# Optimization experiments

Hardware: AMD Instinct MI355X
Metric: run time of the kernel (lower is better)

Reference implementation:

```python
import jax, jax.numpy as jnp
import numpy as np

K = 4          # neighbors
R = 2          # step_ratio
O = 64         # output_size


def setup_inputs() -> dict:
    key = jax.random.key(0)
    ks = jax.random.split(key, 7)
    B, C, N = 16, 128, 2048
    x = jax.random.normal(ks[0], (B, C, N), jnp.float32)
    # 1x1 conv weights stored as [out, in]; bias [out]
    w1 = jax.random.normal(ks[1], (O, 2 * C), jnp.float32) * (1.0 / np.sqrt(2 * C))
    b1 = jax.random.normal(ks[2], (O,), jnp.float32) * 0.01
    w2 = jax.random.normal(ks[3], (O * R, 2 * C + O), jnp.float32) * (1.0 / np.sqrt(2 * C + O))
    b2 = jax.random.normal(ks[4], (O * R,), jnp.float32) * 0.01
    w3 = jax.random.normal(ks[5], (O, O), jnp.float32) * (1.0 / np.sqrt(O))
    b3 = jax.random.normal(ks[6], (O,), jnp.float32) * 0.01
    return {"x": x, "w1": w1, "b1": b1, "w2": w2, "b2": b2, "w3": w3, "b3": b3}


def _knn_idx(x, k):
    # x: [B, C, N]; returns indices of k nearest neighbors (incl. self) [B, N, k]
    inner = -2.0 * jnp.einsum('bcn,bcm->bnm', x, x)           # [B, N, N]
    xx = jnp.sum(x * x, axis=1)                                # [B, N]
    pd = -xx[:, :, None] - inner - xx[:, None, :]              # negative sq dist
    return jax.lax.top_k(pd, k)[1]                             # [B, N, k]


def _graph_feature(x, k):
    # minus_center=False variant used by EF_expansion
    idx = _knn_idx(x, k)                                       # [B, N, k]
    xt = jnp.transpose(x, (0, 2, 1))                           # [B, N, C]
    feat = jax.vmap(lambda xb, ib: xb[ib])(xt, idx)            # [B, N, k, C]
    center = jnp.broadcast_to(xt[:, :, None, :], feat.shape)   # [B, N, k, C]
    f = jnp.concatenate([center, feat], axis=3)                # [B, N, k, 2C]
    return jnp.transpose(f, (0, 3, 1, 2))                      # [B, 2C, N, k]


def _conv1x1(w, b, x):
    # x: [B, Cin, H, W] -> [B, Cout, H, W]
    return jnp.einsum('oc,bchw->bohw', w, x) + b[None, :, None, None]


def reference(x, w1, b1, w2, b2, w3, b3):
    B, C, N = x.shape
    ief = jnp.transpose(_graph_feature(x, K), (0, 1, 3, 2))    # [B, 2C, k, N]
    e1 = _conv1x1(w1, b1, ief)                                 # [B, O, k, N]
    e = jax.nn.relu(jnp.concatenate([e1, ief], axis=1))        # [B, O+2C, k, N]
    e2 = jax.nn.relu(_conv1x1(w2, b2, e))                      # [B, O*R, k, N]
    # [B,O*R,k,N] -> [B,k,N,O*R] -> [B,k,N*R,O] -> [B,O,k,N*R]
    e2 = jnp.transpose(e2, (0, 2, 3, 1)).reshape(B, K, N * R, O)
    e2 = jnp.transpose(e2, (0, 3, 1, 2))
    e3 = _conv1x1(w3, b3, e2)                                  # [B, O, k, N*R]
    return jnp.max(e3, axis=2)                                 # [B, O, N*R]
```

## Files before the change

kernel.cpp:

```cpp
#include <hip/hip_runtime.h>
#include <cstdint>
#include <cstddef>

#define B_  16
#define C_  128
#define N_  2048
#define K_  4
#define O_  64
#define C2_ 256
#define ED_ 320
#define NM_ 4096

typedef float  f32x4  __attribute__((ext_vector_type(4)));
typedef short  s16x8  __attribute__((ext_vector_type(8)));
typedef __bf16 bf16x4 __attribute__((ext_vector_type(4)));
typedef __bf16 bf16x8 __attribute__((ext_vector_type(8)));
typedef unsigned short u16;
typedef unsigned int   u32;
typedef unsigned int   u32x4 __attribute__((ext_vector_type(4)));

__device__ __forceinline__ u32 umin32(u32 a, u32 b) { return a < b ? a : b; }
__device__ __forceinline__ u32 umax32(u32 a, u32 b) { return a > b ? a : b; }

__device__ __forceinline__ s16x8 ldw_bf16(const float* __restrict__ p) {
  float4 a = *(const float4*)p;
  float4 c = *(const float4*)(p + 4);
  bf16x8 r;
  r[0] = (__bf16)a.x; r[1] = (__bf16)a.y; r[2] = (__bf16)a.z; r[3] = (__bf16)a.w;
  r[4] = (__bf16)c.x; r[5] = (__bf16)c.y; r[6] = (__bf16)c.z; r[7] = (__bf16)c.w;
  return __builtin_bit_cast(s16x8, r);
}

__device__ __forceinline__ u32 relu2(u32 u) {
  u32 s = u & 0x80008000u;
  u32 m = s - (s >> 15);
  return u & ~(m | s);
}

__device__ __forceinline__ s16x8 relu8(s16x8 v) {
  u32x4 u = __builtin_bit_cast(u32x4, v);
  u[0] = relu2(u[0]); u[1] = relu2(u[1]);
  u[2] = relu2(u[2]); u[3] = relu2(u[3]);
  return __builtin_bit_cast(s16x8, u);
}

__device__ __forceinline__ void glds16(const void* g, void* l) {
  __builtin_amdgcn_global_load_lds(
      (const __attribute__((address_space(1))) u32*)g,
      (__attribute__((address_space(3))) u32*)l, 16, 0, 0);
}

__global__ __launch_bounds__(256) void prep_kernel(const float* __restrict__ x,
                                                   const float* __restrict__ w1,
                                                   const float* __restrict__ w2,
                                                   const float* __restrict__ w3,
                                                   float* __restrict__ xT32,
                                                   u16* __restrict__ xh,
                                                   float* __restrict__ xx,
                                                   u16* __restrict__ wh) {
  const int t = threadIdx.x;
  if (blockIdx.y == B_) {
    const int gid = blockIdx.x * 256 + t;
    for (int i = gid; i < 15360; i += 8192) {
      const float* src; u16* dst;
      if (i < 4096)       { src = w1 + (size_t)i * 4;            dst = wh + (size_t)i * 4; }
      else if (i < 14336) { src = w2 + (size_t)(i - 4096) * 4;   dst = wh + 16384 + (size_t)(i - 4096) * 4; }
      else                { src = w3 + (size_t)(i - 14336) * 4;  dst = wh + 57344 + (size_t)(i - 14336) * 4; }
      float4 v = *(const float4*)src;
      ushort4 h;
      h.x = __builtin_bit_cast(u16, (__bf16)v.x);
      h.y = __builtin_bit_cast(u16, (__bf16)v.y);
      h.z = __builtin_bit_cast(u16, (__bf16)v.z);
      h.w = __builtin_bit_cast(u16, (__bf16)v.w);
      *(ushort4*)dst = h;
    }
    return;
  }

  __shared__ __align__(16) float sx[C_][65];
  const int b = blockIdx.y, n0 = blockIdx.x * 64;
  const float* xb = x + (size_t)b * C_ * N_;
  for (int u = t; u < C_ * 16; u += 256) {
    int c = u >> 4, f4 = u & 15;
    float4 v = *(const float4*)&xb[(size_t)c * N_ + n0 + f4 * 4];
    sx[c][f4 * 4 + 0] = v.x; sx[c][f4 * 4 + 1] = v.y;
    sx[c][f4 * 4 + 2] = v.z; sx[c][f4 * 4 + 3] = v.w;
  }
  __syncthreads();
  if (t < 64) {
    float s = 0.f;
    for (int c = 0; c < C_; ++c) { float v = sx[c][t]; s = fmaf(v, v, s); }
    xx[b * N_ + n0 + t] = s;
  }
  for (int u = t; u < 64 * 16; u += 256) {
    int n = u >> 4, cb = u & 15;
    float vv[8]; s16x8 hv;
#pragma unroll
    for (int j = 0; j < 8; ++j) {
      float v = sx[cb * 8 + j][n];
      vv[j] = v;
      hv[j] = (short)__builtin_bit_cast(u16, (__bf16)v);
    }
    size_t ro = ((size_t)b * N_ + n0 + n) * C_;
    *(float4*)&xT32[ro + cb * 8]     = make_float4(vv[0], vv[1], vv[2], vv[3]);
    *(float4*)&xT32[ro + cb * 8 + 4] = make_float4(vv[4], vv[5], vv[6], vv[7]);
    int sc = cb ^ (n & 7);
    *(s16x8*)&xh[ro + sc * 8] = hv;
  }
}

__global__ __launch_bounds__(256) void knn_mfma(const u16* __restrict__ xh,
                                                const float* __restrict__ xx,
                                                int* __restrict__ cand8) {
  __shared__ __align__(16) char smem[40960];
  const int b = blockIdx.y, q0 = blockIdx.x * 64;
  const int t = threadIdx.x;
  const int lane = t & 63, wv = t >> 6, lq = t & 15, lh = (t >> 4) & 3;
  const u16* xhb = xh + (size_t)b * N_ * C_;
  const float* xxb = xx + b * N_;

  s16x8 qf[4][4];
#pragma unroll
  for (int qt = 0; qt < 4; ++qt)
#pragma unroll
    for (int ks = 0; ks < 4; ++ks) {
      int q = q0 + qt * 16 + lq;
      int ch = (ks * 4 + lh) ^ (q & 7);
      qf[qt][ks] = *(const s16x8*)&xhb[(size_t)q * C_ + ch * 8];
    }

  u32 pk[4][5];
#pragma unroll
  for (int qt = 0; qt < 4; ++qt)
#pragma unroll
    for (int s = 0; s < 5; ++s) pk[qt][s] = 0xFFFFFFFFu;

  auto stage = [&](int bufi, int m0) {
    const char* s = (const char*)(xhb + (size_t)m0 * C_);
    char* d = smem + bufi * 16384;
#pragma unroll
    for (int c = 0; c < 4; ++c) {
      int off = (wv * 4 + c) * 1024;
      glds16(s + off + lane * 16, d + off);
    }
  };

  stage(0, 0);
  asm volatile("s_waitcnt vmcnt(0)");
  __syncthreads();

  for (int step = 0; step < 32; ++step) {
    const int cur = step & 1;
    if (step < 31) stage(cur ^ 1, (step + 1) * 64);
    const char* mb = smem + cur * 16384;
    f32x4 acc[4];
#pragma unroll
    for (int qt = 0; qt < 4; ++qt) acc[qt] = (f32x4){0.f, 0.f, 0.f, 0.f};
#pragma unroll
    for (int ks = 0; ks < 4; ++ks) {
      int row = wv * 16 + lq;
      int ch = (ks * 4 + lh) ^ (lq & 7);
      s16x8 mf = *(const s16x8*)(mb + row * 256 + ch * 16);
#pragma unroll
      for (int qt = 0; qt < 4; ++qt)
        acc[qt] = __builtin_amdgcn_mfma_f32_16x16x32_bf16(mf, qf[qt][ks], acc[qt], 0, 0, 0);
    }
    const int mrow = step * 64 + wv * 16 + lh * 4;
    float4 xm4 = *(const float4*)&xxb[mrow];
    float xma[4] = {xm4.x, xm4.y, xm4.z, xm4.w};
#pragma unroll
    for (int r = 0; r < 4; ++r) {
#pragma unroll
      for (int qt = 0; qt < 4; ++qt) {
        float dd = fmaf(acc[qt][r], -2.f, xma[r]);
        u32 s = __builtin_bit_cast(u32, dd);
        u32 neg = (u32)((int)s >> 31);
        u32 u = s ^ (neg | 0x80000000u);
        u32 v = (u & 0xFFFFF800u) | (u32)(mrow + r);
#pragma unroll
        for (int s5 = 0; s5 < 5; ++s5) {
          u32 lo = umin32(v, pk[qt][s5]);
          v = umax32(v, pk[qt][s5]);
          pk[qt][s5] = lo;
        }
      }
    }
    asm volatile("s_waitcnt vmcnt(0)");
    __syncthreads();
  }

  u32* cd = (u32*)smem;
  const int unit = wv * 4 + lh;
#pragma unroll
  for (int qt = 0; qt < 4; ++qt) {
    int ql = qt * 16 + lq;
#pragma unroll
    for (int s = 0; s < 5; ++s) cd[ql * 85 + unit * 5 + s] = pk[qt][s];
  }
  __syncthreads();
  if (t < 64) {
    u32 fd[8];
#pragma unroll
    for (int s = 0; s < 8; ++s) fd[s] = 0xFFFFFFFFu;
    for (int j = 0; j < 80; ++j) {
      u32 v = cd[t * 85 + j];
#pragma unroll
      for (int s = 0; s < 8; ++s) {
        u32 lo = umin32(v, fd[s]);
        v = umax32(v, fd[s]);
        fd[s] = lo;
      }
    }
#pragma unroll
    for (int s = 0; s < 8; ++s)
      cand8[((size_t)b * N_ + q0 + t) * 8 + s] = (int)(fd[s] & 0x7FFu);
  }
}

__global__ __launch_bounds__(256) void rerank_kernel(const float* __restrict__ xT32,
                                                     const float* __restrict__ xx,
                                                     const int* __restrict__ cand8,
                                                     int* __restrict__ knn_out) {
  __shared__ __align__(16) float sq[64][132];
  __shared__ float sd[64][8];
  __shared__ int   si[64][8];
  const int b = blockIdx.y, n0 = blockIdx.x * 64;
  const int t = threadIdx.x;
  const float* xb32 = xT32 + (size_t)b * N_ * C_;
  for (int u = t; u < 64 * 32; u += 256) {
    int n = u >> 5, seg = u & 31;
    *(float4*)&sq[n][seg * 4] = *(const float4*)&xb32[(size_t)(n0 + n) * C_ + seg * 4];
  }
  __syncthreads();
  const int ql = t >> 2, cs = t & 3;
#pragma unroll
  for (int cc = 0; cc < 2; ++cc) {
    int cslot = cs + cc * 4;
    int idx = cand8[((size_t)b * N_ + n0 + ql) * 8 + cslot];
    const float* mr = &xb32[(size_t)idx * C_];
    float a0 = 0.f, a1 = 0.f, a2 = 0.f, a3 = 0.f;
#pragma unroll 8
    for (int i = 0; i < 32; ++i) {
      float4 qv = *(const float4*)&sq[ql][i * 4];
      float4 mv = *(const float4*)&mr[i * 4];
      a0 = fmaf(qv.x, mv.x, a0); a1 = fmaf(qv.y, mv.y, a1);
      a2 = fmaf(qv.z, mv.z, a2); a3 = fmaf(qv.w, mv.w, a3);
    }
    float dot = (a0 + a1) + (a2 + a3);
    sd[ql][cslot] = xx[(size_t)b * N_ + idx] - 2.f * dot;
    si[ql][cslot] = idx;
  }
  __syncthreads();
  if (t < 64) {
    float dloc[8]; int iloc[8];
#pragma unroll
    for (int j = 0; j < 8; ++j) { dloc[j] = sd[t][j]; iloc[j] = si[t][j]; }
    u32 used = 0;
#pragma unroll
    for (int s = 0; s < 4; ++s) {
      float bdv = 1e30f; int bidx = 0x7fffffff; int bj = 0;
#pragma unroll
      for (int j = 0; j < 8; ++j) {
        if (!((used >> j) & 1)) {
          bool bet = (dloc[j] < bdv) || (dloc[j] == bdv && iloc[j] < bidx);
          if (bet) { bdv = dloc[j]; bidx = iloc[j]; bj = j; }
        }
      }
      used |= 1u << bj;
      knn_out[((size_t)b * N_ + n0 + t) * K_ + s] = bidx;
    }
  }
}

__global__ __launch_bounds__(256) void xx_kernel(const float* __restrict__ x,
                                                 float* __restrict__ xx) {
  int g = blockIdx.x * 256 + threadIdx.x;
  int b = g >> 11;
  int n = g & (N_ - 1);
  const float* xp = x + (size_t)b * C_ * N_ + n;
  float s = 0.f;
#pragma unroll 8
  for (int c = 0; c < C_; ++c) { float v = xp[(size_t)c * N_]; s += v * v; }
  xx[g] = s;
}

__global__ __launch_bounds__(256) void knn_kernel(const float* __restrict__ x,
                                                  const float* __restrict__ xx,
                                                  int* __restrict__ knn_out) {
  __shared__ __align__(16) float qT[C_ * 64];
  __shared__ __align__(16) float mT[C_ * 64];
  const int b = blockIdx.y;
  const int q0 = blockIdx.x * 64;
  const int t = threadIdx.x;
  const float* xb = x + (size_t)b * C_ * N_;
  const float* xxb = xx + b * N_;
  for (int i = t; i < C_ * 64; i += 256) {
    int c = i >> 6, q = i & 63;
    qT[i] = xb[(size_t)c * N_ + q0 + q];
  }
  const int tq = t & 15;
  const int tm = t >> 4;
  float bd[4][4]; int bi[4][4];
#pragma unroll
  for (int a = 0; a < 4; ++a)
#pragma unroll
    for (int s = 0; s < 4; ++s) { bd[a][s] = 1e30f; bi[a][s] = 0; }
  for (int m0 = 0; m0 < N_; m0 += 64) {
    __syncthreads();
    for (int i = t; i < C_ * 64; i += 256) {
      int c = i >> 6, m = i & 63;
      mT[i] = xb[(size_t)c * N_ + m0 + m];
    }
    __syncthreads();
    float acc[4][4];
#pragma unroll
    for (int a = 0; a < 4; ++a)
#pragma unroll
      for (int j = 0; j < 4; ++j) acc[a][j] = 0.f;
#pragma unroll 4
    for (int c = 0; c < C_; ++c) {
      float4 qv = *(const float4*)&qT[c * 64 + tq * 4];
      float4 mv = *(const float4*)&mT[c * 64 + tm * 4];
      float qa[4] = {qv.x, qv.y, qv.z, qv.w};
      float ma[4] = {mv.x, mv.y, mv.z, mv.w};
#pragma unroll
      for (int a = 0; a < 4; ++a)
#pragma unroll
        for (int j = 0; j < 4; ++j) acc[a][j] += qa[a] * ma[j];
    }
#pragma unroll
    for (int j = 0; j < 4; ++j) {
      float xm = xxb[m0 + tm * 4 + j];
      int id = m0 + tm * 4 + j;
#pragma unroll
      for (int a = 0; a < 4; ++a) {
        float d = xm - 2.f * acc[a][j];
        if (d < bd[a][3]) {
          bd[a][3] = d; bi[a][3] = id;
#pragma unroll
          for (int s = 3; s > 0; --s)
            if (bd[a][s] < bd[a][s - 1]) {
              float td = bd[a][s]; bd[a][s] = bd[a][s - 1]; bd[a][s - 1] = td;
              int ti = bi[a][s]; bi[a][s] = bi[a][s - 1]; bi[a][s - 1] = ti;
            }
        }
      }
    }
  }
  __syncthreads();
  float* cd = qT;
  int* ci = (int*)mT;
#pragma unroll
  for (int a = 0; a < 4; ++a) {
    int q = tq * 4 + a;
#pragma unroll
    for (int s = 0; s < 4; ++s) {
      cd[q * 64 + tm * 4 + s] = bd[a][s];
      ci[q * 64 + tm * 4 + s] = bi[a][s];
    }
  }
  __syncthreads();
  if (t < 64) {
    float fd[4]; int fi[4];
#pragma unroll
    for (int s = 0; s < 4; ++s) { fd[s] = 1e30f; fi[s] = 0; }
    for (int j = 0; j < 64; ++j) {
      float d = cd[t * 64 + j];
      int id = ci[t * 64 + j];
      if (d < fd[3]) {
        fd[3] = d; fi[3] = id;
#pragma unroll
        for (int s = 3; s > 0; --s)
          if (fd[s] < fd[s - 1]) {
            float td = fd[s]; fd[s] = fd[s - 1]; fd[s - 1] = td;
            int ti = fi[s]; fi[s] = fi[s - 1]; fi[s - 1] = ti;
          }
      }
    }
#pragma unroll
    for (int s = 0; s < 4; ++s)
      knn_out[(b * N_ + q0 + t) * K_ + s] = fi[s];
  }
}

__global__ __launch_bounds__(256, 5) void fused_mfma(
    const float* __restrict__ x, const u16* __restrict__ xh,
    const u16* __restrict__ wh, const int* __restrict__ knn_idx,
    const float* __restrict__ w1, const float* __restrict__ b1,
    const float* __restrict__ w2, const float* __restrict__ b2,
    const float* __restrict__ w3, const float* __restrict__ b3,
    float* __restrict__ out) {
  __shared__ __align__(16) char fsm[30976];
  __bf16 (*cT)[136]  = (__bf16(*)[136])(fsm);
  __bf16 (*e1T)[72]  = (__bf16(*)[72])(fsm + 4352);
  float  (*oSt)[36]  = (float(*)[36])(fsm + 4352);
  __bf16 (*nT)[136]  = (__bf16(*)[136])(fsm + 13568);
  __bf16 (*e2T)[136] = (__bf16(*)[136])(fsm + 13568);

  const int b  = blockIdx.y;
  const int n0 = blockIdx.x * 16;
  const int t  = threadIdx.x;
  const float* xb = x + (size_t)b * C_ * N_;
  const u16* xhb = xh ? xh + (size_t)b * N_ * C_ : nullptr;
  const u16* w1h = wh;
  const u16* w2h = wh + 16384;
  const u16* w3h = wh + 57344;

  {
    const int stn = t >> 4, stc = t & 15;
    const int kbase = (b * N_ + n0) * K_;
    if (xhb) {
      int gn = n0 + stn;
      *(s16x8*)&cT[stn][stc * 8] =
          *(const s16x8*)&xhb[(size_t)gn * C_ + ((stc ^ (gn & 7)) * 8)];
#pragma unroll
      for (int it = 0; it < 4; ++it) {
        int col = stn + 16 * it;
        int nid = knn_idx[kbase + col];
        *(s16x8*)&nT[col][stc * 8] =
            *(const s16x8*)&xhb[(size_t)nid * C_ + ((stc ^ (nid & 7)) * 8)];
      }
    } else {
      const float* srcc = xb + (size_t)(stc * 8) * N_ + n0 + stn;
      bf16x8 raw;
#pragma unroll
      for (int j = 0; j < 8; ++j) raw[j] = (__bf16)srcc[(size_t)j * N_];
      *(bf16x8*)&cT[stn][stc * 8] = raw;
#pragma unroll
      for (int it = 0; it < 4; ++it) {
        int col = stn + 16 * it;
        int nid = knn_idx[kbase + col];
        const float* src = xb + (size_t)(stc * 8) * N_ + nid;
        bf16x8 rw;
#pragma unroll
        for (int j = 0; j < 8; ++j) rw[j] = (__bf16)src[(size_t)j * N_];
        *(bf16x8*)&nT[col][stc * 8] = rw;
      }
    }
  }
  __syncthreads();

  const int lq = t & 15;
  const int lh = (t >> 4) & 3;
  const int wv = t >> 6;

  {
    const u16* w1hr = w1h + (size_t)(wv * 16 + lq) * C2_;
    const float* w1r = w1 + (size_t)(wv * 16 + lq) * C2_;
    f32x4 acc[4];
#pragma unroll
    for (int cg = 0; cg < 4; ++cg) acc[cg] = (f32x4){0.f, 0.f, 0.f, 0.f};
#pragma unroll
    for (int ks = 0; ks < 8; ++ks) {
      s16x8 a = wh ? *(const s16x8*)&w1hr[ks * 32 + lh * 8]
                   : ldw_bf16(w1r + ks * 32 + lh * 8);
#pragma unroll
      for (int cg = 0; cg < 4; ++cg) {
        const __bf16* bp = (ks < 4)
            ? &cT[cg * 4 + (lq >> 2)][ks * 32 + lh * 8]
            : &nT[cg * 16 + lq][(ks - 4) * 32 + lh * 8];
        acc[cg] = __builtin_amdgcn_mfma_f32_16x16x32_bf16(
            a, *(const s16x8*)bp, acc[cg], 0, 0, 0);
      }
    }
#pragma unroll
    for (int cg = 0; cg < 4; ++cg) {
      bf16x4 st;
#pragma unroll
      for (int r = 0; r < 4; ++r) {
        float v = acc[cg][r] + b1[wv * 16 + lh * 4 + r];
        st[r] = (__bf16)fmaxf(v, 0.f);
      }
      *(bf16x4*)&e1T[cg * 16 + lq][wv * 16 + lh * 4] = st;
    }
  }
  __syncthreads();

  f32x4 acc2[2][4];
  {
    const u16* w2hr0 = w2h + (size_t)(wv * 32 + lq) * ED_;
    const u16* w2hr1 = w2hr0 + (size_t)16 * ED_;
    const float* w2r0 = w2 + (size_t)(wv * 32 + lq) * ED_;
    const float* w2r1 = w2r0 + (size_t)16 * ED_;
#pragma unroll
    for (int ro = 0; ro < 2; ++ro)
#pragma unroll
      for (int cg = 0; cg < 4; ++cg) acc2[ro][cg] = (f32x4){0.f, 0.f, 0.f, 0.f};
#pragma unroll
    for (int ks = 0; ks < 10; ++ks) {
      s16x8 a0 = wh ? *(const s16x8*)&w2hr0[ks * 32 + lh * 8]
                    : ldw_bf16(w2r0 + ks * 32 + lh * 8);
      s16x8 a1 = wh ? *(const s16x8*)&w2hr1[ks * 32 + lh * 8]
                    : ldw_bf16(w2r1 + ks * 32 + lh * 8);
#pragma unroll
      for (int cg = 0; cg < 4; ++cg) {
        s16x8 bf;
        if (ks < 2)      bf = *(const s16x8*)&e1T[cg * 16 + lq][ks * 32 + lh * 8];
        else if (ks < 6) bf = relu8(*(const s16x8*)&cT[cg * 4 + (lq >> 2)][(ks - 2) * 32 + lh * 8]);
        else             bf = relu8(*(const s16x8*)&nT[cg * 16 + lq][(ks - 6) * 32 + lh * 8]);
        acc2[0][cg] = __builtin_amdgcn_mfma_f32_16x16x32_bf16(a0, bf, acc2[0][cg], 0, 0, 0);
        acc2[1][cg] = __builtin_amdgcn_mfma_f32_16x16x32_bf16(a1, bf, acc2[1][cg], 0, 0, 0);
      }
    }
  }
  __syncthreads();
  {
#pragma unroll
    for (int ro = 0; ro < 2; ++ro)
#pragma unroll
      for (int cg = 0; cg < 4; ++cg) {
        bf16x4 st;
#pragma unroll
        for (int r = 0; r < 4; ++r) {
          float v = acc2[ro][cg][r] + b2[wv * 32 + ro * 16 + lh * 4 + r];
          st[r] = (__bf16)fmaxf(v, 0.f);
        }
        *(bf16x4*)&e2T[cg * 16 + lq][wv * 32 + ro * 16 + lh * 4] = st;
      }
  }
  __syncthreads();

  {
    s16x8 a0, a1;
    if (wh) {
      const u16* w3hr = w3h + (size_t)(wv * 16 + lq) * O_;
      a0 = *(const s16x8*)&w3hr[lh * 8];
      a1 = *(const s16x8*)&w3hr[32 + lh * 8];
    } else {
      const float* w3r = w3 + (size_t)(wv * 16 + lq) * O_;
      a0 = ldw_bf16(w3r + lh * 8);
      a1 = ldw_bf16(w3r + 32 + lh * 8);
    }
#pragma unroll
    for (int cg = 0; cg < 8; ++cg) {
      int col = cg * 16 + lq;
      int nl = col >> 3, rr = (col >> 2) & 1, kk = col & 3;
      const __bf16* base = &e2T[nl * 4 + kk][rr * 64];
      f32x4 acc = {0.f, 0.f, 0.f, 0.f};
      acc = __builtin_amdgcn_mfma_f32_16x16x32_bf16(a0, *(const s16x8*)(base + lh * 8),      acc, 0, 0, 0);
      acc = __builtin_amdgcn_mfma_f32_16x16x32_bf16(a1, *(const s16x8*)(base + 32 + lh * 8), acc, 0, 0, 0);
      float vv[4];
#pragma unroll
      for (int r = 0; r < 4; ++r) {
        float v = acc[r];
        v = fmaxf(v, __shfl_xor(v, 1));
        v = fmaxf(v, __shfl_xor(v, 2));
        vv[r] = v;
      }
      if ((lq & 3) == 0) {
        int mloc = col >> 2;
        int o = wv * 16 + lh * 4;
#pragma unroll
        for (int r = 0; r < 4; ++r) oSt[o + r][mloc] = vv[r] + b3[o + r];
      }
    }
  }
  __syncthreads();

#pragma unroll
  for (int it = 0; it < 2; ++it) {
    int u = t + it * 256;
    int o = u >> 3, seg = u & 7;
    *(float4*)&out[((size_t)b * O_ + o) * NM_ + n0 * 2 + seg * 4] =
        *(const float4*)&oSt[o][seg * 4];
  }
}

extern "C" void kernel_launch(void* const* d_in, const int* in_sizes, int n_in,
                              void* d_out, int out_size, void* d_ws, size_t ws_size,
                              hipStream_t stream) {
  const float* x  = (const float*)d_in[0];
  const float* w1 = (const float*)d_in[1];
  const float* b1 = (const float*)d_in[2];
  const float* w2 = (const float*)d_in[3];
  const float* b2 = (const float*)d_in[4];
  const float* w3 = (const float*)d_in[5];
  const float* b3 = (const float*)d_in[6];
  float* out = (float*)d_out;

  const size_t off_xh   = (size_t)B_ * N_ * C_ * 4;
  const size_t off_xx   = off_xh + (size_t)B_ * N_ * C_ * 2;
  const size_t off_c8   = off_xx + (size_t)B_ * N_ * 4;
  const size_t off_knn  = off_c8 + (size_t)B_ * N_ * 8 * 4;
  const size_t off_wh   = off_knn + (size_t)B_ * N_ * K_ * 4;
  const size_t NEED     = off_wh + (size_t)61440 * 2;

  if (ws_size >= NEED) {
    float* xT32 = (float*)d_ws;
    u16*   xhp  = (u16*)((char*)d_ws + off_xh);
    float* xx   = (float*)((char*)d_ws + off_xx);
    int*   c8   = (int*)((char*)d_ws + off_c8);
    int*   knn  = (int*)((char*)d_ws + off_knn);
    u16*   whp  = (u16*)((char*)d_ws + off_wh);

    hipLaunchKernelGGL(prep_kernel, dim3(N_ / 64, B_ + 1), dim3(256), 0, stream,
                       x, w1, w2, w3, xT32, xhp, xx, whp);
    hipLaunchKernelGGL(knn_mfma, dim3(N_ / 64, B_), dim3(256), 0, stream, xhp, xx, c8);
    hipLaunchKernelGGL(rerank_kernel, dim3(N_ / 64, B_), dim3(256), 0, stream, xT32, xx, c8, knn);
    hipLaunchKernelGGL(fused_mfma, dim3(N_ / 16, B_), dim3(256), 0, stream,
                       x, xhp, whp, knn, w1, b1, w2, b2, w3, b3, out);
  } else {
    float* xx = (float*)d_ws;
    int* knn = (int*)((char*)d_ws + (size_t)B_ * N_ * 4);
    hipLaunchKernelGGL(xx_kernel, dim3((B_ * N_) / 256), dim3(256), 0, stream, x, xx);
    hipLaunchKernelGGL(knn_kernel, dim3(N_ / 64, B_), dim3(256), 0, stream, x, xx, knn);
    hipLaunchKernelGGL(fused_mfma, dim3(N_ / 16, B_), dim3(256), 0, stream,
                       x, (const u16*)nullptr, (const u16*)nullptr, knn,
                       w1, b1, w2, b2, w3, b3, out);
  }
}
```

Baseline: 119.1 us.

## Add persistent tiled fused kernel with register-resident weights and async LDS double buffering

Introduces fused_tiled, where each block handles 64 points in four 16-point iterations. The block loads the bf16 weight fragments for all three convs into registers once, instead of reloading them per 16-point block. Center and neighbor rows are staged into double-buffered LDS with global_load_lds using an XOR swizzle, so the gather for the next tile overlaps compute on the current one. This cuts redundant weight traffic and gather latency, at the cost of heavy register pressure (launch bounds 256,2), more LDS per block, and lower occupancy.

```diff
diff --git a/kernel.cpp b/kernel.cpp
--- a/kernel.cpp
+++ b/kernel.cpp
@@ -10,6 +10,7 @@
 #define C2_ 256
 #define ED_ 320
 #define NM_ 4096
+#define ROWB 256
 
 typedef float  f32x4  __attribute__((ext_vector_type(4)));
 typedef short  s16x8  __attribute__((ext_vector_type(8)));
@@ -36,7 +37,6 @@
   u32 m = s - (s >> 15);
   return u & ~(m | s);
 }
-
 __device__ __forceinline__ s16x8 relu8(s16x8 v) {
   u32x4 u = __builtin_bit_cast(u32x4, v);
   u[0] = relu2(u[0]); u[1] = relu2(u[1]);
@@ -272,6 +272,195 @@
   }
 }
 
+__global__ __launch_bounds__(256, 2) void fused_tiled(
+    const u16* __restrict__ xh, const u16* __restrict__ wh,
+    const int* __restrict__ knn_idx,
+    const float* __restrict__ b1, const float* __restrict__ b2,
+    const float* __restrict__ b3, float* __restrict__ out) {
+  __shared__ __align__(16) char fsm[66560];
+  __bf16* e1T = (__bf16*)(fsm + 40960);
+  float*  oSt = (float*)(fsm + 40960);
+  char*   e2T = fsm + 50176;
+
+  const int t  = threadIdx.x;
+  const int lane = t & 63, wv = t >> 6, lq = t & 15, lh = (t >> 4) & 3;
+  const int b = blockIdx.y;
+  const int nbase = blockIdx.x * 64;
+  const u16* xhb = xh + (size_t)b * N_ * C_;
+  const int kb = (b * N_ + nbase) * K_;
+
+  s16x8 w1f[8], w2f0[10], w2f1[10], w3f[2];
+  {
+    const u16* r1 = wh + (size_t)(wv * 16 + lq) * C2_;
+#pragma unroll
+    for (int ks = 0; ks < 8; ++ks) w1f[ks] = *(const s16x8*)&r1[ks * 32 + lh * 8];
+    const u16* r20 = wh + 16384 + (size_t)(wv * 32 + lq) * ED_;
+    const u16* r21 = r20 + (size_t)16 * ED_;
+#pragma unroll
+    for (int ks = 0; ks < 10; ++ks) {
+      w2f0[ks] = *(const s16x8*)&r20[ks * 32 + lh * 8];
+      w2f1[ks] = *(const s16x8*)&r21[ks * 32 + lh * 8];
+    }
+    const u16* r3 = wh + 57344 + (size_t)(wv * 16 + lq) * O_;
+    w3f[0] = *(const s16x8*)&r3[lh * 8];
+    w3f[1] = *(const s16x8*)&r3[32 + lh * 8];
+  }
+  const float4 b1v  = *(const float4*)&b1[wv * 16 + lh * 4];
+  const float4 b2v0 = *(const float4*)&b2[wv * 32 + lh * 4];
+  const float4 b2v1 = *(const float4*)&b2[wv * 32 + 16 + lh * 4];
+  const float4 b3v  = *(const float4*)&b3[wv * 16 + lh * 4];
+
+  auto stageTile = [&](int it, const int* nids) {
+    char* cb = fsm + (it & 1) * 20480;
+    char* nb = cb + 4096;
+    glds16((const char*)xhb + (size_t)(nbase + it * 16 + wv * 4) * ROWB + lane * 16,
+           cb + wv * 4 * ROWB);
+#pragma unroll
+    for (int g = 0; g < 4; ++g) {
+      int col = wv * 16 + g * 4 + (lane >> 4);
+      int nid = nids[g];
+      int sc = (lane & 15) ^ (col & 7) ^ (nid & 7);
+      glds16((const char*)xhb + (size_t)nid * ROWB + sc * 16,
+             nb + (wv * 16 + g * 4) * ROWB);
+    }
+  };
+
+  int nids[4];
+#pragma unroll
+  for (int g = 0; g < 4; ++g)
+    nids[g] = knn_idx[kb + wv * 16 + g * 4 + (lane >> 4)];
+  stageTile(0, nids);
+
+  for (int it = 0; it < 4; ++it) {
+    if (it < 3) {
+#pragma unroll
+      for (int g = 0; g < 4; ++g)
+        nids[g] = knn_idx[kb + (it + 1) * 64 + wv * 16 + g * 4 + (lane >> 4)];
+    }
+    asm volatile("s_waitcnt vmcnt(0)" ::: "memory");
+    __syncthreads();
+    if (it < 3) stageTile(it + 1, nids);
+
+    const char* cb = fsm + (it & 1) * 20480;
+    const char* nb = cb + 4096;
+
+    {
+      f32x4 acc1[4];
+#pragma unroll
+      for (int cg = 0; cg < 4; ++cg) acc1[cg] = (f32x4){0.f, 0.f, 0.f, 0.f};
+#pragma unroll
+      for (int ks = 0; ks < 8; ++ks) {
+#pragma unroll
+        for (int cg = 0; cg < 4; ++cg) {
+          const char* bp;
+          if (ks < 4) {
+            int r = cg * 4 + (lq >> 2);
+            bp = cb + r * ROWB + (((ks * 4 + lh) ^ (r & 7)) * 16);
+          } else {
+            int r = cg * 16 + lq;
+            bp = nb + r * ROWB + ((((ks - 4) * 4 + lh) ^ (r & 7)) * 16);
+          }
+          acc1[cg] = __builtin_amdgcn_mfma_f32_16x16x32_bf16(
+              w1f[ks], *(const s16x8*)bp, acc1[cg], 0, 0, 0);
+        }
+      }
+      const float bb[4] = {b1v.x, b1v.y, b1v.z, b1v.w};
+#pragma unroll
+      for (int cg = 0; cg < 4; ++cg) {
+        bf16x4 st;
+#pragma unroll
+        for (int r = 0; r < 4; ++r) st[r] = (__bf16)fmaxf(acc1[cg][r] + bb[r], 0.f);
+        *(bf16x4*)&e1T[(cg * 16 + lq) * 72 + wv * 16 + lh * 4] = st;
+      }
+    }
+    __syncthreads();
+
+    {
+      f32x4 acc2[2][4];
+#pragma unroll
+      for (int ro = 0; ro < 2; ++ro)
+#pragma unroll
+        for (int cg = 0; cg < 4; ++cg) acc2[ro][cg] = (f32x4){0.f, 0.f, 0.f, 0.f};
+#pragma unroll
+      for (int ks = 0; ks < 10; ++ks) {
+#pragma unroll
+        for (int cg = 0; cg < 4; ++cg) {
+          s16x8 bf;
+          if (ks < 2) {
+            bf = *(const s16x8*)&e1T[(cg * 16 + lq) * 72 + ks * 32 + lh * 8];
+          } else if (ks < 6) {
+            int r = cg * 4 + (lq >> 2);
+            bf = relu8(*(const s16x8*)(cb + r * ROWB + ((((ks - 2) * 4 + lh) ^ (r & 7)) * 16)));
+          } else {
+            int r = cg * 16 + lq;
+            bf = relu8(*(const s16x8*)(nb + r * ROWB + ((((ks - 6) * 4 + lh) ^ (r & 7)) * 16)));
+          }
+          acc2[0][cg] = __builtin_amdgcn_mfma_f32_16x16x32_bf16(w2f0[ks], bf, acc2[0][cg], 0, 0, 0);
+          acc2[1][cg] = __builtin_amdgcn_mfma_f32_16x16x32_bf16(w2f1[ks], bf, acc2[1][cg], 0, 0, 0);
+        }
+      }
+      const float c0[4] = {b2v0.x, b2v0.y, b2v0.z, b2v0.w};
+      const float c1[4] = {b2v1.x, b2v1.y, b2v1.z, b2v1.w};
+#pragma unroll
+      for (int ro = 0; ro < 2; ++ro)
+#pragma unroll
+        for (int cg = 0; cg < 4; ++cg) {
+          int col = cg * 16 + lq;
+          int e = wv * 32 + ro * 16 + lh * 4;
+          int j = e >> 3, sub = e & 7;
+          int pos = j ^ (col & 7);
+          bf16x4 st;
+#pragma unroll
+          for (int r = 0; r < 4; ++r) {
+            float v = acc2[ro][cg][r] + (ro ? c1[r] : c0[r]);
+            st[r] = (__bf16)fmaxf(v, 0.f);
+          }
+          *(bf16x4*)(e2T + col * ROWB + pos * 16 + sub * 2) = st;
+        }
+    }
+    __syncthreads();
+
+    {
+#pragma unroll
+      for (int cg = 0; cg < 8; ++cg) {
+        int col = cg * 16 + lq;
+        int nl = col >> 3, rr = (col >> 2) & 1, kk = col & 3;
+        int row = nl * 4 + kk;
+        int j1 = rr * 8 + lh, j2 = rr * 8 + 4 + lh;
+        s16x8 f1 = *(const s16x8*)(e2T + row * ROWB + ((j1 ^ (row & 7)) * 16));
+        s16x8 f2 = *(const s16x8*)(e2T + row * ROWB + ((j2 ^ (row & 7)) * 16));
+        f32x4 acc = {0.f, 0.f, 0.f, 0.f};
+        acc = __builtin_amdgcn_mfma_f32_16x16x32_bf16(w3f[0], f1, acc, 0, 0, 0);
+        acc = __builtin_amdgcn_mfma_f32_16x16x32_bf16(w3f[1], f2, acc, 0, 0, 0);
+        float vv[4];
+#pragma unroll
+        for (int r = 0; r < 4; ++r) {
+          float v = acc[r];
+          v = fmaxf(v, __shfl_xor(v, 1));
+          v = fmaxf(v, __shfl_xor(v, 2));
+          vv[r] = v;
+        }
+        if ((lq & 3) == 0) {
+          int mloc = col >> 2;
+          int o = wv * 16 + lh * 4;
+          const float b3a[4] = {b3v.x, b3v.y, b3v.z, b3v.w};
+#pragma unroll
+          for (int r = 0; r < 4; ++r) oSt[(o + r) * 36 + mloc] = vv[r] + b3a[r];
+        }
+      }
+    }
+    __syncthreads();
+
+#pragma unroll
+    for (int io = 0; io < 2; ++io) {
+      int u = t + io * 256;
+      int o = u >> 3, seg = u & 7;
+      *(float4*)&out[((size_t)b * O_ + o) * NM_ + nbase * 2 + it * 32 + seg * 4] =
+          *(const float4*)&oSt[o * 36 + seg * 4];
+    }
+  }
+}
+
 __global__ __launch_bounds__(256) void xx_kernel(const float* __restrict__ x,
                                                  float* __restrict__ xx) {
   int g = blockIdx.x * 256 + threadIdx.x;
@@ -383,9 +572,8 @@
   }
 }
 
-__global__ __launch_bounds__(256, 5) void fused_mfma(
-    const float* __restrict__ x, const u16* __restrict__ xh,
-    const u16* __restrict__ wh, const int* __restrict__ knn_idx,
+__global__ __launch_bounds__(256, 5) void fused_fb(
+    const float* __restrict__ x, const int* __restrict__ knn_idx,
     const float* __restrict__ w1, const float* __restrict__ b1,
     const float* __restrict__ w2, const float* __restrict__ b2,
     const float* __restrict__ w3, const float* __restrict__ b3,
@@ -401,41 +589,24 @@
   const int n0 = blockIdx.x * 16;
   const int t  = threadIdx.x;
   const float* xb = x + (size_t)b * C_ * N_;
-  const u16* xhb = xh ? xh + (size_t)b * N_ * C_ : nullptr;
-  const u16* w1h = wh;
-  const u16* w2h = wh + 16384;
-  const u16* w3h = wh + 57344;
 
   {
     const int stn = t >> 4, stc = t & 15;
     const int kbase = (b * N_ + n0) * K_;
-    if (xhb) {
-      int gn = n0 + stn;
-      *(s16x8*)&cT[stn][stc * 8] =
-          *(const s16x8*)&xhb[(size_t)gn * C_ + ((stc ^ (gn & 7)) * 8)];
-#pragma unroll
-      for (int it = 0; it < 4; ++it) {
-        int col = stn + 16 * it;
-        int nid = knn_idx[kbase + col];
-        *(s16x8*)&nT[col][stc * 8] =
-            *(const s16x8*)&xhb[(size_t)nid * C_ + ((stc ^ (nid & 7)) * 8)];
-      }
-    } else {
-      const float* srcc = xb + (size_t)(stc * 8) * N_ + n0 + stn;
-      bf16x8 raw;
-#pragma unroll
-      for (int j = 0; j < 8; ++j) raw[j] = (__bf16)srcc[(size_t)j * N_];
-      *(bf16x8*)&cT[stn][stc * 8] = raw;
-#pragma unroll
-      for (int it = 0; it < 4; ++it) {
-        int col = stn + 16 * it;
-        int nid = knn_idx[kbase + col];
-        const float* src = xb + (size_t)(stc * 8) * N_ + nid;
-        bf16x8 rw;
-#pragma unroll
-        for (int j = 0; j < 8; ++j) rw[j] = (__bf16)src[(size_t)j * N_];
-        *(bf16x8*)&nT[col][stc * 8] = rw;
-      }
+    const float* srcc = xb + (size_t)(stc * 8) * N_ + n0 + stn;
+    bf16x8 raw;
+#pragma unroll
+    for (int j = 0; j < 8; ++j) raw[j] = (__bf16)srcc[(size_t)j * N_];
+    *(bf16x8*)&cT[stn][stc * 8] = raw;
+#pragma unroll
+    for (int it = 0; it < 4; ++it) {
+      int col = stn + 16 * it;
+      int nid = knn_idx[kbase + col];
+      const float* src = xb + (size_t)(stc * 8) * N_ + nid;
+      bf16x8 rw;
+#pragma unroll
+      for (int j = 0; j < 8; ++j) rw[j] = (__bf16)src[(size_t)j * N_];
+      *(bf16x8*)&nT[col][stc * 8] = rw;
     }
   }
   __syncthreads();
@@ -445,15 +616,13 @@
   const int wv = t >> 6;
 
   {
-    const u16* w1hr = w1h + (size_t)(wv * 16 + lq) * C2_;
     const float* w1r = w1 + (size_t)(wv * 16 + lq) * C2_;
     f32x4 acc[4];
 #pragma unroll
     for (int cg = 0; cg < 4; ++cg) acc[cg] = (f32x4){0.f, 0.f, 0.f, 0.f};
 #pragma unroll
     for (int ks = 0; ks < 8; ++ks) {
-      s16x8 a = wh ? *(const s16x8*)&w1hr[ks * 32 + lh * 8]
-                   : ldw_bf16(w1r + ks * 32 + lh * 8);
+      s16x8 a = ldw_bf16(w1r + ks * 32 + lh * 8);
 #pragma unroll
       for (int cg = 0; cg < 4; ++cg) {
         const __bf16* bp = (ks < 4)
@@ -478,8 +647,6 @@
 
   f32x4 acc2[2][4];
   {
-    const u16* w2hr0 = w2h + (size_t)(wv * 32 + lq) * ED_;
-    const u16* w2hr1 = w2hr0 + (size_t)16 * ED_;
     const float* w2r0 = w2 + (size_t)(wv * 32 + lq) * ED_;
     const float* w2r1 = w2r0 + (size_t)16 * ED_;
 #pragma unroll
@@ -488,10 +655,8 @@
       for (int cg = 0; cg < 4; ++cg) acc2[ro][cg] = (f32x4){0.f, 0.f, 0.f, 0.f};
 #pragma unroll
     for (int ks = 0; ks < 10; ++ks) {
-      s16x8 a0 = wh ? *(const s16x8*)&w2hr0[ks * 32 + lh * 8]
-                    : ldw_bf16(w2r0 + ks * 32 + lh * 8);
-      s16x8 a1 = wh ? *(const s16x8*)&w2hr1[ks * 32 + lh * 8]
-                    : ldw_bf16(w2r1 + ks * 32 + lh * 8);
+      s16x8 a0 = ldw_bf16(w2r0 + ks * 32 + lh * 8);
+      s16x8 a1 = ldw_bf16(w2r1 + ks * 32 + lh * 8);
 #pragma unroll
       for (int cg = 0; cg < 4; ++cg) {
         s16x8 bf;
@@ -521,16 +686,9 @@
   __syncthreads();
 
   {
-    s16x8 a0, a1;
-    if (wh) {
-      const u16* w3hr = w3h + (size_t)(wv * 16 + lq) * O_;
-      a0 = *(const s16x8*)&w3hr[lh * 8];
-      a1 = *(const s16x8*)&w3hr[32 + lh * 8];
-    } else {
-      const float* w3r = w3 + (size_t)(wv * 16 + lq) * O_;
-      a0 = ldw_bf16(w3r + lh * 8);
-      a1 = ldw_bf16(w3r + 32 + lh * 8);
-    }
+    const float* w3r = w3 + (size_t)(wv * 16 + lq) * O_;
+    s16x8 a0 = ldw_bf16(w3r + lh * 8);
+    s16x8 a1 = ldw_bf16(w3r + 32 + lh * 8);
 #pragma unroll
     for (int cg = 0; cg < 8; ++cg) {
       int col = cg * 16 + lq;
@@ -597,15 +755,14 @@
                        x, w1, w2, w3, xT32, xhp, xx, whp);
     hipLaunchKernelGGL(knn_mfma, dim3(N_ / 64, B_), dim3(256), 0, stream, xhp, xx, c8);
     hipLaunchKernelGGL(rerank_kernel, dim3(N_ / 64, B_), dim3(256), 0, stream, xT32, xx, c8, knn);
-    hipLaunchKernelGGL(fused_mfma, dim3(N_ / 16, B_), dim3(256), 0, stream,
-                       x, xhp, whp, knn, w1, b1, w2, b2, w3, b3, out);
+    hipLaunchKernelGGL(fused_tiled, dim3(N_ / 64, B_), dim3(256), 0, stream,
+                       xhp, whp, knn, b1, b2, b3, out);
   } else {
     float* xx = (float*)d_ws;
     int* knn = (int*)((char*)d_ws + (size_t)B_ * N_ * 4);
     hipLaunchKernelGGL(xx_kernel, dim3((B_ * N_) / 256), dim3(256), 0, stream, x, xx);
     hipLaunchKernelGGL(knn_kernel, dim3(N_ / 64, B_), dim3(256), 0, stream, x, xx, knn);
-    hipLaunchKernelGGL(fused_mfma, dim3(N_ / 16, B_), dim3(256), 0, stream,
-                       x, (const u16*)nullptr, (const u16*)nullptr, knn,
-                       w1, b1, w2, b2, w3, b3, out);
-  }
-}
+    hipLaunchKernelGGL(fused_fb, dim3(N_ / 16, B_), dim3(256), 0, stream,
+                       x, knn, w1, b1, w2, b2, w3, b3, out);
+  }
+}
```

Result: slower. 124.9 us (+4.9%).
